# Optimization experiments

Measured on AMD Instinct MI355X. Metric: run time of the kernel, lower is better.

## Reference

```python
import jax, jax.numpy as jnp
import numpy as np

# --- grid constants (from init_kwargs) ---
VOXEL = jnp.array([0.2, 0.2, 6.0], dtype=jnp.float32)
PC_MIN = jnp.array([-51.2, -51.2, -3.0], dtype=jnp.float32)
PC_MAX = jnp.array([51.2, 51.2, 3.0], dtype=jnp.float32)
NY, NX = 512, 512          # pseudo_image_dims
NSEG = NY * NX             # dense pillar grid used as segment space
BN_EPS = 1e-3


def setup_inputs() -> dict:
    key = jax.random.key(0)
    k1, k2 = jax.random.split(key)
    B, N, C = 2, 100000, 64
    # points roughly spanning the range, slightly beyond so some get filtered
    pts = jax.random.uniform(k1, (B, N, 3), dtype=jnp.float32)
    lo = jnp.array([-56.0, -56.0, -3.5], dtype=jnp.float32)
    hi = jnp.array([56.0, 56.0, 3.5], dtype=jnp.float32)
    points = lo + pts * (hi - lo)
    W = jax.random.normal(k2, (9, C), dtype=jnp.float32) * 0.1
    return {
        "points": points,
        "W": W,
        "gamma": jnp.ones((C,), jnp.float32),
        "beta": jnp.zeros((C,), jnp.float32),
        "running_mean": jnp.zeros((C,), jnp.float32),
        "running_var": jnp.ones((C,), jnp.float32),
    }


def _embed_one(pts, W, gamma, beta, r_mean, r_var):
    # pts: [N,3] -> pseudo-image [C, NY, NX]
    coords = jnp.floor((pts - PC_MIN) / VOXEL).astype(jnp.int32)        # [N,3] (x,y,z)
    in_range = jnp.all((pts >= PC_MIN) & (pts < PC_MAX), axis=-1)       # [N]
    pid = coords[:, 1] * NX + coords[:, 0]                              # pillar id = y*nx + x
    pid = jnp.where(in_range, pid, 0)
    w = in_range.astype(pts.dtype)[:, None]                             # [N,1] mask weight

    cnt = jax.ops.segment_sum(w[:, 0], pid, num_segments=NSEG)          # [NSEG]
    safe_cnt = jnp.maximum(cnt, 1.0)

    # cluster center offset: per-pillar mean of xyz
    sum_xyz = jax.ops.segment_sum(pts * w, pid, num_segments=NSEG)      # [NSEG,3]
    mean_xyz = sum_xyz / safe_cnt[:, None]
    f_cluster = pts - mean_xyz[pid]

    # voxel center offset
    center = (coords.astype(pts.dtype) + 0.5) * VOXEL + PC_MIN
    f_center = pts - center

    feats = jnp.concatenate([pts, f_cluster, f_center], axis=-1)        # [N,9]

    # PFN layer: Linear(9->C, no bias) + BN1d (eval, running stats) + ReLU
    h = feats @ W                                                       # [N,C]
    h = (h - r_mean) * jax.lax.rsqrt(r_var + BN_EPS) * gamma + beta
    h = jax.nn.relu(h)

    # scatter-avg per pillar, then dense canvas
    vsum = jax.ops.segment_sum(h * w, pid, num_segments=NSEG)           # [NSEG,C]
    vfeat = vsum / safe_cnt[:, None]
    return vfeat.reshape(NY, NX, -1).transpose(2, 0, 1)                 # [C,NY,NX]


def reference(points, W, gamma, beta, running_mean, running_var):
    # points: [B,N,3] -> pseudo-image [B,C,NY,NX]
    return jax.vmap(_embed_one, in_axes=(0, None, None, None, None, None))(
        points, W, gamma, beta, running_mean, running_var)
```

## Files before the change

kernel.cpp:

```cpp
#include <hip/hip_runtime.h>
#include <math.h>

#define NXg 512
#define NYg 512
#define NSEG (NXg * NYg)
#define CCH 64
#define CAP 16
#define ECAP 15
#define SLOTS 4
#define PSTR 5
#define PPB 64
#define BN_EPS 1e-3f

#define PCMINX (-51.2f)
#define PCMINY (-51.2f)
#define PCMINZ (-3.0f)
#define PCMAXX (51.2f)
#define PCMAXY (51.2f)
#define PCMAXZ (3.0f)
#define VOXX (0.2f)
#define VOXY (0.2f)
#define VOXZ (6.0f)

#define RECIPX 5.0f
#define RECIPY 5.0f
#define RECIPZ (__uint_as_float(0x3E2AAAABu))

__device__ __forceinline__ int calc_pid(float x, float y, float z) {
    bool in_range = (x >= PCMINX) && (x < PCMAXX) &&
                    (y >= PCMINY) && (y < PCMAXY) &&
                    (z >= PCMINZ) && (z < PCMAXZ);
    if (!in_range) return -1;
    int cx = (int)floorf((x - PCMINX) * RECIPX);
    int cy = (int)floorf((y - PCMINY) * RECIPY);
    int p = cy * NXg + cx;
    return (p >= 0 && p < NSEG) ? p : -1;
}

__global__ void k1_bin(const float* __restrict__ pts, unsigned* __restrict__ cnt,
                       float4* __restrict__ first, float4* __restrict__ ext,
                       int B, int N) {
    int i = blockIdx.x * blockDim.x + threadIdx.x;
    if (i >= B * N) return;
    const float* p = pts + (size_t)i * 3;
    float x = p[0], y = p[1], z = p[2];
    int pd = calc_pid(x, y, z);
    if (pd < 0) return;
    int b = i / N;
    int g = b * NSEG + pd;
    unsigned slot = atomicAdd(&cnt[g], 1u);
    float4 e; e.x = x; e.y = y; e.z = z; e.w = 0.0f;
    if (slot == 0) first[g] = e;
    else if (slot < CAP) ext[(size_t)g * ECAP + (slot - 1)] = e;
}

__global__ void __launch_bounds__(256) k4_compute(
    const unsigned* __restrict__ cnt, const float4* __restrict__ first,
    const float4* __restrict__ ext,
    const float* __restrict__ W, const float* __restrict__ gamma,
    const float* __restrict__ beta, const float* __restrict__ rmean,
    const float* __restrict__ rvar, float* __restrict__ out) {
    __shared__ float pxs[PPB * PSTR];
    __shared__ float pys[PPB * PSTR];
    __shared__ float pzs[PPB * PSTR];
    __shared__ float mxs[PPB], mys[PPB], mzs[PPB];
    __shared__ int ks[PPB];
    __shared__ float tile[CCH * 65];

    int t = threadIdx.x;
    int lane = t & 63;
    int wave = t >> 6;
    int gp0 = blockIdx.x * PPB;

    float w0 = W[0 * CCH + lane], w1 = W[1 * CCH + lane], w2 = W[2 * CCH + lane];
    float w3 = W[3 * CCH + lane], w4 = W[4 * CCH + lane], w5 = W[5 * CCH + lane];
    float w6 = W[6 * CCH + lane], w7 = W[7 * CCH + lane], w8 = W[8 * CCH + lane];
    float sc = gamma[lane] * (1.0f / sqrtf(rvar[lane] + BN_EPS));
    float shift = beta[lane] - rmean[lane] * sc;
    float Ac = (w0 + w3 + w6) * sc;
    float Bc = (w1 + w4 + w7) * sc;
    float Cc = (w2 + w5) * sc;
    float s3 = w3 * sc, s4 = w4 * sc, s5 = w5 * sc;
    float s6 = w6 * sc, s7 = w7 * sc, s8 = w8 * sc;

    if (t < PPB) {
        int gp = gp0 + t;
        float4 f0 = first[gp];
        unsigned kc = cnt[gp];
        int k = (kc < CAP) ? (int)kc : CAP;
        ks[t] = k;
        float sx = 0.f, sy = 0.f, sz = 0.f;
        if (k > 0) {
            sx = f0.x; sy = f0.y; sz = f0.z;
            pxs[t * PSTR + 0] = f0.x;
            pys[t * PSTR + 0] = f0.y;
            pzs[t * PSTR + 0] = f0.z;
            const float4* ex = ext + (size_t)gp * ECAP;
            for (int j = 1; j < k; ++j) {
                float4 e = ex[j - 1];
                if (j < SLOTS) {
                    pxs[t * PSTR + j] = e.x;
                    pys[t * PSTR + j] = e.y;
                    pzs[t * PSTR + j] = e.z;
                }
                sx += e.x; sy += e.y; sz += e.z;
            }
        }
        float fk = (k > 0) ? (float)k : 1.0f;
        mxs[t] = sx / fk; mys[t] = sy / fk; mzs[t] = sz / fk;
    }
    __syncthreads();

    for (int it = 0; it < 16; ++it) {
        int ppl = wave * 16 + it;
        int k = ks[ppl];
        float acc = 0.0f;
        if (k > 0) {
            float mx = mxs[ppl], my = mys[ppl], mz = mzs[ppl];
            int pid = (gp0 + ppl) & (NSEG - 1);
            float ctx = ((float)(pid & (NXg - 1)) + 0.5f) * VOXX + PCMINX;
            float cty = ((float)(pid >> 9) + 0.5f) * VOXY + PCMINY;
            float D = shift;
            D = fmaf(-mx, s3, D); D = fmaf(-my, s4, D); D = fmaf(-mz, s5, D);
            D = fmaf(-ctx, s6, D); D = fmaf(-cty, s7, D);
            int kl = (k < SLOTS) ? k : SLOTS;
            for (int j = 0; j < kl; ++j) {
                float x = pxs[ppl * PSTR + j];
                float y = pys[ppl * PSTR + j];
                float z = pzs[ppl * PSTR + j];
                float cz = floorf((z - PCMINZ) * RECIPZ);
                float ctz = (cz + 0.5f) * VOXZ + PCMINZ;
                float h = fmaf(x, Ac, fmaf(y, Bc, fmaf(z, Cc, fmaf(z - ctz, s8, D))));
                acc += fmaxf(h, 0.0f);
            }
            for (int j = SLOTS; j < k; ++j) {
                float4 e = ext[(size_t)(gp0 + ppl) * ECAP + (j - 1)];
                float cz = floorf((e.z - PCMINZ) * RECIPZ);
                float ctz = (cz + 0.5f) * VOXZ + PCMINZ;
                float h = fmaf(e.x, Ac, fmaf(e.y, Bc, fmaf(e.z, Cc,
                              fmaf(e.z - ctz, s8, D))));
                acc += fmaxf(h, 0.0f);
            }
            acc /= (float)k;
        }
        tile[lane * 65 + ppl] = acc;
    }
    __syncthreads();

    int b = gp0 >> 18;
    int pbatch = gp0 & (NSEG - 1);
    size_t obase = (size_t)b * CCH * NSEG + (size_t)pbatch;
    for (int jj = 0; jj < 4; ++jj) {
        int idx = jj * 256 + t;
        int c = idx >> 4;
        int q = idx & 15;
        float4 v;
        v.x = tile[c * 65 + q * 4 + 0];
        v.y = tile[c * 65 + q * 4 + 1];
        v.z = tile[c * 65 + q * 4 + 2];
        v.w = tile[c * 65 + q * 4 + 3];
        *reinterpret_cast<float4*>(out + obase + (size_t)c * NSEG + q * 4) = v;
    }
}

extern "C" void kernel_launch(void* const* d_in, const int* in_sizes, int n_in,
                              void* d_out, int out_size, void* d_ws, size_t ws_size,
                              hipStream_t stream) {
    const float* points = (const float*)d_in[0];
    const float* W      = (const float*)d_in[1];
    const float* gamma  = (const float*)d_in[2];
    const float* beta   = (const float*)d_in[3];
    const float* rmean  = (const float*)d_in[4];
    const float* rvar   = (const float*)d_in[5];
    float* out = (float*)d_out;

    int B = out_size / (CCH * NSEG);
    int N = in_sizes[0] / (3 * B);
    int BN = B * NSEG;
    int total_pts = B * N;

    unsigned* cnt = (unsigned*)d_ws;
    float4* first = (float4*)(cnt + BN);
    float4* ext   = first + BN;

    hipMemsetAsync(cnt, 0, (size_t)BN * sizeof(unsigned), stream);

    int blk = 256;
    int grd_pts = (total_pts + blk - 1) / blk;
    k1_bin<<<grd_pts, blk, 0, stream>>>(points, cnt, first, ext, B, N);
    k4_compute<<<BN / PPB, blk, 0, stream>>>(cnt, first, ext, W, gamma, beta,
                                             rmean, rvar, out);
}
```

Baseline: 47.89 us.

## Map one pillar per thread and loop channels with coalesced direct stores

The compute kernel now gives each thread one pillar and loops over all 64 channels, writing each channel plane directly with coalesced stores. This removes the shared-memory staging, the two block barriers and the transpose tile. A new init kernel zeroes the counters in place of the memset and precomputes the folded weight/BN coefficient table once, so blocks no longer redo that setup. In exchange each thread holds more registers, and warps where pillars have uneven point counts diverge on the per-point branches.

Measured after the change: 56.00 us. 16.9% more time.

```diff
diff --git a/kernel.cpp b/kernel.cpp
--- a/kernel.cpp
+++ b/kernel.cpp
@@ -7,9 +7,6 @@
 #define CCH 64
 #define CAP 16
 #define ECAP 15
-#define SLOTS 4
-#define PSTR 5
-#define PPB 64
 #define BN_EPS 1e-3f
 
 #define PCMINX (-51.2f)
@@ -37,6 +34,36 @@
     return (p >= 0 && p < NSEG) ? p : -1;
 }
 
+__global__ void k0_init(unsigned* __restrict__ cnt, float* __restrict__ cTab,
+                        const float* __restrict__ W,
+                        const float* __restrict__ gamma,
+                        const float* __restrict__ beta,
+                        const float* __restrict__ rmean,
+                        const float* __restrict__ rvar, int BN) {
+    int i = blockIdx.x * blockDim.x + threadIdx.x;
+    if (i < BN) cnt[i] = 0u;
+    if (blockIdx.x == 0 && threadIdx.x < CCH) {
+        int c = threadIdx.x;
+        float w0 = W[0 * CCH + c], w1 = W[1 * CCH + c], w2 = W[2 * CCH + c];
+        float w3 = W[3 * CCH + c], w4 = W[4 * CCH + c], w5 = W[5 * CCH + c];
+        float w6 = W[6 * CCH + c], w7 = W[7 * CCH + c], w8 = W[8 * CCH + c];
+        float sc = gamma[c] * (1.0f / sqrtf(rvar[c] + BN_EPS));
+        float shift = beta[c] - rmean[c] * sc;
+        cTab[c * 12 + 0] = (w0 + w3 + w6) * sc;
+        cTab[c * 12 + 1] = (w1 + w4 + w7) * sc;
+        cTab[c * 12 + 2] = (w2 + w5) * sc;
+        cTab[c * 12 + 3] = w8 * sc;
+        cTab[c * 12 + 4] = w3 * sc;
+        cTab[c * 12 + 5] = w4 * sc;
+        cTab[c * 12 + 6] = w5 * sc;
+        cTab[c * 12 + 7] = w6 * sc;
+        cTab[c * 12 + 8] = w7 * sc;
+        cTab[c * 12 + 9] = shift;
+        cTab[c * 12 + 10] = 0.0f;
+        cTab[c * 12 + 11] = 0.0f;
+    }
+}
+
 __global__ void k1_bin(const float* __restrict__ pts, unsigned* __restrict__ cnt,
                        float4* __restrict__ first, float4* __restrict__ ext,
                        int B, int N) {
@@ -54,112 +81,88 @@
     else if (slot < CAP) ext[(size_t)g * ECAP + (slot - 1)] = e;
 }
 
+__device__ __forceinline__ float zcenter_off(float z) {
+    float cz = floorf((z - PCMINZ) * RECIPZ);
+    float ctz = (cz + 0.5f) * VOXZ + PCMINZ;
+    return z - ctz;
+}
+
 __global__ void __launch_bounds__(256) k4_compute(
     const unsigned* __restrict__ cnt, const float4* __restrict__ first,
-    const float4* __restrict__ ext,
-    const float* __restrict__ W, const float* __restrict__ gamma,
-    const float* __restrict__ beta, const float* __restrict__ rmean,
-    const float* __restrict__ rvar, float* __restrict__ out) {
-    __shared__ float pxs[PPB * PSTR];
-    __shared__ float pys[PPB * PSTR];
-    __shared__ float pzs[PPB * PSTR];
-    __shared__ float mxs[PPB], mys[PPB], mzs[PPB];
-    __shared__ int ks[PPB];
-    __shared__ float tile[CCH * 65];
+    const float4* __restrict__ ext, const float4* __restrict__ cTab4,
+    float* __restrict__ out) {
+    int t = threadIdx.x;
+    int gp = (int)blockIdx.x * 256 + t;
 
-    int t = threadIdx.x;
-    int lane = t & 63;
-    int wave = t >> 6;
-    int gp0 = blockIdx.x * PPB;
+    float4 f0 = first[gp];
+    unsigned kc = cnt[gp];
+    int k = (kc < CAP) ? (int)kc : CAP;
+    const float4* ex = ext + (size_t)gp * ECAP;
 
-    float w0 = W[0 * CCH + lane], w1 = W[1 * CCH + lane], w2 = W[2 * CCH + lane];
-    float w3 = W[3 * CCH + lane], w4 = W[4 * CCH + lane], w5 = W[5 * CCH + lane];
-    float w6 = W[6 * CCH + lane], w7 = W[7 * CCH + lane], w8 = W[8 * CCH + lane];
-    float sc = gamma[lane] * (1.0f / sqrtf(rvar[lane] + BN_EPS));
-    float shift = beta[lane] - rmean[lane] * sc;
-    float Ac = (w0 + w3 + w6) * sc;
-    float Bc = (w1 + w4 + w7) * sc;
-    float Cc = (w2 + w5) * sc;
-    float s3 = w3 * sc, s4 = w4 * sc, s5 = w5 * sc;
-    float s6 = w6 * sc, s7 = w7 * sc, s8 = w8 * sc;
+    float x0 = 0.f, y0 = 0.f, z0 = 0.f;
+    float x1 = 0.f, y1 = 0.f, z1 = 0.f;
+    float x2 = 0.f, y2 = 0.f, z2 = 0.f;
+    float x3 = 0.f, y3 = 0.f, z3 = 0.f;
+    float sx = 0.f, sy = 0.f, sz = 0.f;
+    if (k > 0) { x0 = f0.x; y0 = f0.y; z0 = f0.z; sx = x0; sy = y0; sz = z0; }
+    if (k > 1) { float4 e = ex[0]; x1 = e.x; y1 = e.y; z1 = e.z;
+                 sx += x1; sy += y1; sz += z1; }
+    if (k > 2) { float4 e = ex[1]; x2 = e.x; y2 = e.y; z2 = e.z;
+                 sx += x2; sy += y2; sz += z2; }
+    if (k > 3) { float4 e = ex[2]; x3 = e.x; y3 = e.y; z3 = e.z;
+                 sx += x3; sy += y3; sz += z3; }
+    for (int j = 4; j < k; ++j) {
+        float4 e = ex[j - 1];
+        sx += e.x; sy += e.y; sz += e.z;
+    }
+    float fk = (k > 0) ? (float)k : 1.0f;
+    float mx = sx / fk, my = sy / fk, mz = sz / fk;
+    float rk = 1.0f / fk;
 
-    if (t < PPB) {
-        int gp = gp0 + t;
-        float4 f0 = first[gp];
-        unsigned kc = cnt[gp];
-        int k = (kc < CAP) ? (int)kc : CAP;
-        ks[t] = k;
-        float sx = 0.f, sy = 0.f, sz = 0.f;
+    float zc0 = zcenter_off(z0), zc1 = zcenter_off(z1);
+    float zc2 = zcenter_off(z2), zc3 = zcenter_off(z3);
+
+    int pid = gp & (NSEG - 1);
+    float ctx = ((float)(pid & (NXg - 1)) + 0.5f) * VOXX + PCMINX;
+    float cty = ((float)(pid >> 9) + 0.5f) * VOXY + PCMINY;
+    size_t ob = (size_t)(gp >> 18) * CCH * NSEG + (size_t)pid;
+
+    for (int c = 0; c < CCH; ++c) {
+        float4 q0 = cTab4[c * 3 + 0];
+        float4 q1 = cTab4[c * 3 + 1];
+        float4 q2 = cTab4[c * 3 + 2];
+        float D = q2.y;
+        D = fmaf(-mx, q1.x, D); D = fmaf(-my, q1.y, D); D = fmaf(-mz, q1.z, D);
+        D = fmaf(-ctx, q1.w, D); D = fmaf(-cty, q2.x, D);
+        float a = 0.0f;
         if (k > 0) {
-            sx = f0.x; sy = f0.y; sz = f0.z;
-            pxs[t * PSTR + 0] = f0.x;
-            pys[t * PSTR + 0] = f0.y;
-            pzs[t * PSTR + 0] = f0.z;
-            const float4* ex = ext + (size_t)gp * ECAP;
-            for (int j = 1; j < k; ++j) {
-                float4 e = ex[j - 1];
-                if (j < SLOTS) {
-                    pxs[t * PSTR + j] = e.x;
-                    pys[t * PSTR + j] = e.y;
-                    pzs[t * PSTR + j] = e.z;
-                }
-                sx += e.x; sy += e.y; sz += e.z;
-            }
+            float h = fmaf(x0, q0.x, fmaf(y0, q0.y, fmaf(z0, q0.z,
+                          fmaf(zc0, q0.w, D))));
+            a += fmaxf(h, 0.0f);
         }
-        float fk = (k > 0) ? (float)k : 1.0f;
-        mxs[t] = sx / fk; mys[t] = sy / fk; mzs[t] = sz / fk;
-    }
-    __syncthreads();
-
-    for (int it = 0; it < 16; ++it) {
-        int ppl = wave * 16 + it;
-        int k = ks[ppl];
-        float acc = 0.0f;
-        if (k > 0) {
-            float mx = mxs[ppl], my = mys[ppl], mz = mzs[ppl];
-            int pid = (gp0 + ppl) & (NSEG - 1);
-            float ctx = ((float)(pid & (NXg - 1)) + 0.5f) * VOXX + PCMINX;
-            float cty = ((float)(pid >> 9) + 0.5f) * VOXY + PCMINY;
-            float D = shift;
-            D = fmaf(-mx, s3, D); D = fmaf(-my, s4, D); D = fmaf(-mz, s5, D);
-            D = fmaf(-ctx, s6, D); D = fmaf(-cty, s7, D);
-            int kl = (k < SLOTS) ? k : SLOTS;
-            for (int j = 0; j < kl; ++j) {
-                float x = pxs[ppl * PSTR + j];
-                float y = pys[ppl * PSTR + j];
-                float z = pzs[ppl * PSTR + j];
-                float cz = floorf((z - PCMINZ) * RECIPZ);
-                float ctz = (cz + 0.5f) * VOXZ + PCMINZ;
-                float h = fmaf(x, Ac, fmaf(y, Bc, fmaf(z, Cc, fmaf(z - ctz, s8, D))));
-                acc += fmaxf(h, 0.0f);
-            }
-            for (int j = SLOTS; j < k; ++j) {
-                float4 e = ext[(size_t)(gp0 + ppl) * ECAP + (j - 1)];
-                float cz = floorf((e.z - PCMINZ) * RECIPZ);
-                float ctz = (cz + 0.5f) * VOXZ + PCMINZ;
-                float h = fmaf(e.x, Ac, fmaf(e.y, Bc, fmaf(e.z, Cc,
-                              fmaf(e.z - ctz, s8, D))));
-                acc += fmaxf(h, 0.0f);
-            }
-            acc /= (float)k;
+        if (k > 1) {
+            float h = fmaf(x1, q0.x, fmaf(y1, q0.y, fmaf(z1, q0.z,
+                          fmaf(zc1, q0.w, D))));
+            a += fmaxf(h, 0.0f);
         }
-        tile[lane * 65 + ppl] = acc;
-    }
-    __syncthreads();
-
-    int b = gp0 >> 18;
-    int pbatch = gp0 & (NSEG - 1);
-    size_t obase = (size_t)b * CCH * NSEG + (size_t)pbatch;
-    for (int jj = 0; jj < 4; ++jj) {
-        int idx = jj * 256 + t;
-        int c = idx >> 4;
-        int q = idx & 15;
-        float4 v;
-        v.x = tile[c * 65 + q * 4 + 0];
-        v.y = tile[c * 65 + q * 4 + 1];
-        v.z = tile[c * 65 + q * 4 + 2];
-        v.w = tile[c * 65 + q * 4 + 3];
-        *reinterpret_cast<float4*>(out + obase + (size_t)c * NSEG + q * 4) = v;
+        if (k > 2) {
+            float h = fmaf(x2, q0.x, fmaf(y2, q0.y, fmaf(z2, q0.z,
+                          fmaf(zc2, q0.w, D))));
+            a += fmaxf(h, 0.0f);
+        }
+        if (k > 3) {
+            float h = fmaf(x3, q0.x, fmaf(y3, q0.y, fmaf(z3, q0.z,
+                          fmaf(zc3, q0.w, D))));
+            a += fmaxf(h, 0.0f);
+        }
+        for (int j = 4; j < k; ++j) {
+            float4 e = ex[j - 1];
+            float zc = zcenter_off(e.z);
+            float h = fmaf(e.x, q0.x, fmaf(e.y, q0.y, fmaf(e.z, q0.z,
+                          fmaf(zc, q0.w, D))));
+            a += fmaxf(h, 0.0f);
+        }
+        out[ob + (size_t)c * NSEG] = a * rk;
     }
 }
 
@@ -180,14 +183,15 @@
     int total_pts = B * N;
 
     unsigned* cnt = (unsigned*)d_ws;
-    float4* first = (float4*)(cnt + BN);
+    float* cTab   = (float*)(cnt + BN);
+    float4* first = (float4*)(cTab + 1024);
     float4* ext   = first + BN;
 
-    hipMemsetAsync(cnt, 0, (size_t)BN * sizeof(unsigned), stream);
-
     int blk = 256;
+    k0_init<<<(BN + blk - 1) / blk, blk, 0, stream>>>(cnt, cTab, W, gamma,
+                                                      beta, rmean, rvar, BN);
     int grd_pts = (total_pts + blk - 1) / blk;
     k1_bin<<<grd_pts, blk, 0, stream>>>(points, cnt, first, ext, B, N);
-    k4_compute<<<BN / PPB, blk, 0, stream>>>(cnt, first, ext, W, gamma, beta,
-                                             rmean, rvar, out);
+    k4_compute<<<BN / 256, blk, 0, stream>>>(cnt, first, ext,
+                                             (const float4*)cTab, out);
 }
```

## Warp-specialize compute kernel with double-buffered pillar gather across tiles

Applied to the files above, without the earlier changes.

Each block now handles four 64-pillar tiles instead of one. The fourth wave acts as a producer that gathers the next tile's point data into a second shared-memory buffer while the other three waves compute the current tile. The aim is to overlap the latency of the global gathers with compute and to amortise the per-block weight setup. In exchange, only three waves do the compute, there are extra barriers per tile, and the grid is four times smaller, which lowers parallelism.

New measurement: 55.03 us. 1.15x slower.

```diff
diff --git a/kernel.cpp b/kernel.cpp
--- a/kernel.cpp
+++ b/kernel.cpp
@@ -10,6 +10,7 @@
 #define SLOTS 4
 #define PSTR 5
 #define PPB 64
+#define TPB 4
 #define BN_EPS 1e-3f
 
 #define PCMINX (-51.2f)
@@ -60,17 +61,17 @@
     const float* __restrict__ W, const float* __restrict__ gamma,
     const float* __restrict__ beta, const float* __restrict__ rmean,
     const float* __restrict__ rvar, float* __restrict__ out) {
-    __shared__ float pxs[PPB * PSTR];
-    __shared__ float pys[PPB * PSTR];
-    __shared__ float pzs[PPB * PSTR];
-    __shared__ float mxs[PPB], mys[PPB], mzs[PPB];
-    __shared__ int ks[PPB];
-    __shared__ float tile[CCH * 65];
+    __shared__ float pxs[2][PPB * PSTR];
+    __shared__ float pys[2][PPB * PSTR];
+    __shared__ float pzs[2][PPB * PSTR];
+    __shared__ float mxs[2][PPB], mys[2][PPB], mzs[2][PPB];
+    __shared__ int ks[2][PPB];
+    __shared__ float tileb[CCH * 65];
 
     int t = threadIdx.x;
     int lane = t & 63;
     int wave = t >> 6;
-    int gp0 = blockIdx.x * PPB;
+    int tile0 = (int)blockIdx.x * TPB;
 
     float w0 = W[0 * CCH + lane], w1 = W[1 * CCH + lane], w2 = W[2 * CCH + lane];
     float w3 = W[3 * CCH + lane], w4 = W[4 * CCH + lane], w5 = W[5 * CCH + lane];
@@ -83,83 +84,97 @@
     float s3 = w3 * sc, s4 = w4 * sc, s5 = w5 * sc;
     float s6 = w6 * sc, s7 = w7 * sc, s8 = w8 * sc;
 
-    if (t < PPB) {
-        int gp = gp0 + t;
+    auto gather = [&](int tile, int buf, int gl) {
+        int gp = tile * PPB + gl;
         float4 f0 = first[gp];
         unsigned kc = cnt[gp];
         int k = (kc < CAP) ? (int)kc : CAP;
-        ks[t] = k;
+        ks[buf][gl] = k;
         float sx = 0.f, sy = 0.f, sz = 0.f;
         if (k > 0) {
             sx = f0.x; sy = f0.y; sz = f0.z;
-            pxs[t * PSTR + 0] = f0.x;
-            pys[t * PSTR + 0] = f0.y;
-            pzs[t * PSTR + 0] = f0.z;
+            pxs[buf][gl * PSTR + 0] = f0.x;
+            pys[buf][gl * PSTR + 0] = f0.y;
+            pzs[buf][gl * PSTR + 0] = f0.z;
             const float4* ex = ext + (size_t)gp * ECAP;
             for (int j = 1; j < k; ++j) {
                 float4 e = ex[j - 1];
                 if (j < SLOTS) {
-                    pxs[t * PSTR + j] = e.x;
-                    pys[t * PSTR + j] = e.y;
-                    pzs[t * PSTR + j] = e.z;
+                    pxs[buf][gl * PSTR + j] = e.x;
+                    pys[buf][gl * PSTR + j] = e.y;
+                    pzs[buf][gl * PSTR + j] = e.z;
                 }
                 sx += e.x; sy += e.y; sz += e.z;
             }
         }
         float fk = (k > 0) ? (float)k : 1.0f;
-        mxs[t] = sx / fk; mys[t] = sy / fk; mzs[t] = sz / fk;
-    }
+        mxs[buf][gl] = sx / fk; mys[buf][gl] = sy / fk; mzs[buf][gl] = sz / fk;
+    };
+
+    if (t >= 192) gather(tile0, 0, t - 192);
     __syncthreads();
 
-    for (int it = 0; it < 16; ++it) {
-        int ppl = wave * 16 + it;
-        int k = ks[ppl];
-        float acc = 0.0f;
-        if (k > 0) {
-            float mx = mxs[ppl], my = mys[ppl], mz = mzs[ppl];
-            int pid = (gp0 + ppl) & (NSEG - 1);
-            float ctx = ((float)(pid & (NXg - 1)) + 0.5f) * VOXX + PCMINX;
-            float cty = ((float)(pid >> 9) + 0.5f) * VOXY + PCMINY;
-            float D = shift;
-            D = fmaf(-mx, s3, D); D = fmaf(-my, s4, D); D = fmaf(-mz, s5, D);
-            D = fmaf(-ctx, s6, D); D = fmaf(-cty, s7, D);
-            int kl = (k < SLOTS) ? k : SLOTS;
-            for (int j = 0; j < kl; ++j) {
-                float x = pxs[ppl * PSTR + j];
-                float y = pys[ppl * PSTR + j];
-                float z = pzs[ppl * PSTR + j];
-                float cz = floorf((z - PCMINZ) * RECIPZ);
-                float ctz = (cz + 0.5f) * VOXZ + PCMINZ;
-                float h = fmaf(x, Ac, fmaf(y, Bc, fmaf(z, Cc, fmaf(z - ctz, s8, D))));
-                acc += fmaxf(h, 0.0f);
+    for (int i = 0; i < TPB; ++i) {
+        int buf = i & 1;
+        int gp0 = (tile0 + i) * PPB;
+
+        if (t >= 192) {
+            if (i + 1 < TPB) gather(tile0 + i + 1, buf ^ 1, t - 192);
+        } else {
+            int pstart = wave * 22;
+            int pend = (wave == 2) ? PPB : pstart + 22;
+            for (int ppl = pstart; ppl < pend; ++ppl) {
+                int k = ks[buf][ppl];
+                float acc = 0.0f;
+                if (k > 0) {
+                    float mx = mxs[buf][ppl], my = mys[buf][ppl], mz = mzs[buf][ppl];
+                    int pid = (gp0 + ppl) & (NSEG - 1);
+                    float ctx = ((float)(pid & (NXg - 1)) + 0.5f) * VOXX + PCMINX;
+                    float cty = ((float)(pid >> 9) + 0.5f) * VOXY + PCMINY;
+                    float D = shift;
+                    D = fmaf(-mx, s3, D); D = fmaf(-my, s4, D); D = fmaf(-mz, s5, D);
+                    D = fmaf(-ctx, s6, D); D = fmaf(-cty, s7, D);
+                    int kl = (k < SLOTS) ? k : SLOTS;
+                    for (int j = 0; j < kl; ++j) {
+                        float x = pxs[buf][ppl * PSTR + j];
+                        float y = pys[buf][ppl * PSTR + j];
+                        float z = pzs[buf][ppl * PSTR + j];
+                        float cz = floorf((z - PCMINZ) * RECIPZ);
+                        float ctz = (cz + 0.5f) * VOXZ + PCMINZ;
+                        float h = fmaf(x, Ac, fmaf(y, Bc, fmaf(z, Cc,
+                                      fmaf(z - ctz, s8, D))));
+                        acc += fmaxf(h, 0.0f);
+                    }
+                    for (int j = SLOTS; j < k; ++j) {
+                        float4 e = ext[(size_t)(gp0 + ppl) * ECAP + (j - 1)];
+                        float cz = floorf((e.z - PCMINZ) * RECIPZ);
+                        float ctz = (cz + 0.5f) * VOXZ + PCMINZ;
+                        float h = fmaf(e.x, Ac, fmaf(e.y, Bc, fmaf(e.z, Cc,
+                                      fmaf(e.z - ctz, s8, D))));
+                        acc += fmaxf(h, 0.0f);
+                    }
+                    acc /= (float)k;
+                }
+                tileb[lane * 65 + ppl] = acc;
             }
-            for (int j = SLOTS; j < k; ++j) {
-                float4 e = ext[(size_t)(gp0 + ppl) * ECAP + (j - 1)];
-                float cz = floorf((e.z - PCMINZ) * RECIPZ);
-                float ctz = (cz + 0.5f) * VOXZ + PCMINZ;
-                float h = fmaf(e.x, Ac, fmaf(e.y, Bc, fmaf(e.z, Cc,
-                              fmaf(e.z - ctz, s8, D))));
-                acc += fmaxf(h, 0.0f);
-            }
-            acc /= (float)k;
         }
-        tile[lane * 65 + ppl] = acc;
-    }
-    __syncthreads();
-
-    int b = gp0 >> 18;
-    int pbatch = gp0 & (NSEG - 1);
-    size_t obase = (size_t)b * CCH * NSEG + (size_t)pbatch;
-    for (int jj = 0; jj < 4; ++jj) {
-        int idx = jj * 256 + t;
-        int c = idx >> 4;
-        int q = idx & 15;
-        float4 v;
-        v.x = tile[c * 65 + q * 4 + 0];
-        v.y = tile[c * 65 + q * 4 + 1];
-        v.z = tile[c * 65 + q * 4 + 2];
-        v.w = tile[c * 65 + q * 4 + 3];
-        *reinterpret_cast<float4*>(out + obase + (size_t)c * NSEG + q * 4) = v;
+        __syncthreads();
+
+        int b = gp0 >> 18;
+        int pbatch = gp0 & (NSEG - 1);
+        size_t obase = (size_t)b * CCH * NSEG + (size_t)pbatch;
+        for (int jj = 0; jj < 4; ++jj) {
+            int idx = jj * 256 + t;
+            int c = idx >> 4;
+            int q = idx & 15;
+            float4 v;
+            v.x = tileb[c * 65 + q * 4 + 0];
+            v.y = tileb[c * 65 + q * 4 + 1];
+            v.z = tileb[c * 65 + q * 4 + 2];
+            v.w = tileb[c * 65 + q * 4 + 3];
+            *reinterpret_cast<float4*>(out + obase + (size_t)c * NSEG + q * 4) = v;
+        }
+        __syncthreads();
     }
 }
 
@@ -188,6 +203,7 @@
     int blk = 256;
     int grd_pts = (total_pts + blk - 1) / blk;
     k1_bin<<<grd_pts, blk, 0, stream>>>(points, cnt, first, ext, B, N);
-    k4_compute<<<BN / PPB, blk, 0, stream>>>(cnt, first, ext, W, gamma, beta,
-                                             rmean, rvar, out);
-}
+    int ntiles = BN / PPB;
+    k4_compute<<<ntiles / TPB, blk, 0, stream>>>(cnt, first, ext, W, gamma,
+                                                 beta, rmean, rvar, out);
+}
```
